# Kernel optimization log

Hardware: AMD Instinct MI355X
Metric: run time of the kernel (lower is better)

The kernel has to match this reference:

```python
import jax, jax.numpy as jnp
import numpy as np

BATCH = 1048576
IN_DIM = 64   # input_dim = A.shape[1]
OUT_DIM = 16  # output_dim = A.shape[0]


def setup_inputs() -> dict:
    key = jax.random.key(0)
    k1, k2, k3 = jax.random.split(key, 3)
    y = jax.random.normal(k1, (BATCH, IN_DIM), dtype=jnp.float32)
    A = jax.random.normal(k2, (OUT_DIM, IN_DIM), dtype=jnp.float32)
    b = jax.random.normal(k3, (BATCH, OUT_DIM), dtype=jnp.float32)
    return {"y": y, "A": A, "b": b}


def _block_matrix(A):
    # KKT block matrix [[2I, A^T], [A, 0]], shape (n+m, n+m); shared across batch.
    m, n = A.shape
    Id2 = 2.0 * jnp.eye(n, dtype=A.dtype)
    top = jnp.concatenate([Id2, A.T], axis=1)          # (n, n+m)
    bot = jnp.concatenate([A, jnp.zeros((m, m), A.dtype)], axis=1)  # (m, n+m)
    return jnp.concatenate([top, bot], axis=0)


def reference(y, A, b):
    # Solve block_matrix @ sol_i = [2*y_i; b_i] for all samples i in one batched solve
    # (original torch code loops torch.linalg.solve over the batch with the SAME matrix).
    n = A.shape[1]
    M = _block_matrix(A)                               # (n+m, n+m)
    rhs = jnp.concatenate([2.0 * y, b], axis=1)        # (batch, n+m)
    sol = jnp.linalg.solve(M, rhs.T).T                 # factorize once, all RHS at once
    y_star = sol[:, :n]
    return y_star
```

## Files before the change

kernel.cpp:

```cpp
#include <hip/hip_runtime.h>

#define BATCH   1048576
#define IN_DIM  64
#define OUT_DIM 16

__global__ __launch_bounds__(256) void precompute_kernel(
    const float* __restrict__ A, float* __restrict__ ws)
{
    __shared__ float sA[16][64];
    __shared__ float M[16][32];
    __shared__ float fac[16];
    __shared__ int piv;

    const int tid = threadIdx.x;

    for (int i = tid; i < 1024; i += 256) sA[i >> 6][i & 63] = A[i];
    __syncthreads();

    {
        const int i = tid >> 4, j = tid & 15;
        float s = 0.f;
        #pragma unroll
        for (int k = 0; k < 64; ++k) s = fmaf(sA[i][k], sA[j][k], s);
        M[i][j] = s;
        M[i][16 + j] = (i == j) ? 1.f : 0.f;
    }
    __syncthreads();

    for (int p = 0; p < 16; ++p) {
        if (tid == 0) {
            int best = p;
            float bv = fabsf(M[p][p]);
            for (int r = p + 1; r < 16; ++r) {
                float v = fabsf(M[r][p]);
                if (v > bv) { bv = v; best = r; }
            }
            piv = best;
        }
        __syncthreads();
        if (tid < 32) {
            const int pr = piv;
            if (pr != p) { float t = M[p][tid]; M[p][tid] = M[pr][tid]; M[pr][tid] = t; }
        }
        __syncthreads();
        const float pv = M[p][p];
        __syncthreads();
        if (tid < 32) M[p][tid] *= (1.0f / pv);
        __syncthreads();
        if (tid < 16) fac[tid] = M[tid][p];
        __syncthreads();
        for (int e = tid; e < 512; e += 256) {
            const int r = e >> 5, c = e & 31;
            if (r != p) M[r][c] = fmaf(-fac[r], M[p][c], M[r][c]);
        }
        __syncthreads();
    }

    for (int e = tid; e < 1024; e += 256) {
        const int k = e >> 4, j = e & 15;
        ws[e] = sA[j][k];
    }
    for (int e = tid; e < 1024; e += 256) {
        const int k = e >> 4, i = e & 15;
        float s = 0.f;
        #pragma unroll
        for (int j = 0; j < 16; ++j) s = fmaf(M[i][16 + j], sA[j][k], s);
        ws[1024 + e] = s;
    }
}

__global__ __launch_bounds__(256, 2) void apply_kernel(
    const float* __restrict__ y, const float* __restrict__ b,
    const float* __restrict__ ws, float* __restrict__ out)
{
    __shared__ float4 yT[4][64][16];

    const int tid = threadIdx.x;
    const int wv  = tid >> 6;
    const int l   = tid & 63;
    const size_t wbase = (size_t)blockIdx.x * 256 + (size_t)wv * 64;

    const float4* __restrict__ At4  = reinterpret_cast<const float4*>(ws);
    const float4* __restrict__ Ct4  = reinterpret_cast<const float4*>(ws + 1024);
    const float4* __restrict__ ysrc = reinterpret_cast<const float4*>(y) + wbase * 16;
    const float4* __restrict__ b4   = reinterpret_cast<const float4*>(b);
    float4* __restrict__ odst       = reinterpret_cast<float4*>(out) + wbase * 16;

    #pragma unroll
    for (int i = 0; i < 16; ++i) {
        const int f   = i * 64 + l;
        const int row = f >> 4, q = f & 15;
        yT[wv][row][q ^ (row & 15)] = ysrc[f];
    }

    float t[16];
    #pragma unroll
    for (int q = 0; q < 4; ++q) {
        const float4 bv = b4[(wbase + l) * 4 + q];
        t[4*q+0] = -bv.x; t[4*q+1] = -bv.y; t[4*q+2] = -bv.z; t[4*q+3] = -bv.w;
    }

    #pragma unroll
    for (int q = 0; q < 16; ++q) {
        const float4 yv = yT[wv][l][q ^ (l & 15)];
        #pragma unroll
        for (int dk = 0; dk < 4; ++dk) {
            const float yk = (dk == 0) ? yv.x : (dk == 1) ? yv.y :
                             (dk == 2) ? yv.z : yv.w;
            const int k = q * 4 + dk;
            #pragma unroll
            for (int jq = 0; jq < 4; ++jq) {
                const float4 a = At4[k * 4 + jq];
                t[4*jq+0] = fmaf(a.x, yk, t[4*jq+0]);
                t[4*jq+1] = fmaf(a.y, yk, t[4*jq+1]);
                t[4*jq+2] = fmaf(a.z, yk, t[4*jq+2]);
                t[4*jq+3] = fmaf(a.w, yk, t[4*jq+3]);
            }
        }
    }

    #pragma unroll
    for (int q = 0; q < 16; ++q) {
        float4 yv = yT[wv][l][q ^ (l & 15)];
        #pragma unroll
        for (int dk = 0; dk < 4; ++dk) {
            const int k = q * 4 + dk;
            float x = (dk == 0) ? yv.x : (dk == 1) ? yv.y :
                      (dk == 2) ? yv.z : yv.w;
            #pragma unroll
            for (int iq = 0; iq < 4; ++iq) {
                const float4 c = Ct4[k * 4 + iq];
                x = fmaf(-c.x, t[4*iq+0], x);
                x = fmaf(-c.y, t[4*iq+1], x);
                x = fmaf(-c.z, t[4*iq+2], x);
                x = fmaf(-c.w, t[4*iq+3], x);
            }
            if (dk == 0) yv.x = x; else if (dk == 1) yv.y = x;
            else if (dk == 2) yv.z = x; else yv.w = x;
        }
        yT[wv][l][q ^ (l & 15)] = yv;
    }

    #pragma unroll
    for (int i = 0; i < 16; ++i) {
        const int f   = i * 64 + l;
        const int row = f >> 4, q = f & 15;
        odst[f] = yT[wv][row][q ^ (row & 15)];
    }
}

extern "C" void kernel_launch(void* const* d_in, const int* in_sizes, int n_in,
                              void* d_out, int out_size, void* d_ws, size_t ws_size,
                              hipStream_t stream) {
    const float* y = (const float*)d_in[0];
    const float* A = (const float*)d_in[1];
    const float* b = (const float*)d_in[2];
    float* out = (float*)d_out;
    float* ws  = (float*)d_ws;

    precompute_kernel<<<1, 256, 0, stream>>>(A, ws);
    apply_kernel<<<BATCH / 256, 256, 0, stream>>>(y, b, ws, out);
}
```

Baseline: 163.7 us.

## Halve apply kernel LDS staging by processing y in two column halves

```diff
diff --git a/kernel.cpp b/kernel.cpp
--- a/kernel.cpp
+++ b/kernel.cpp
@@ -69,40 +69,50 @@
     }
 }
 
-__global__ __launch_bounds__(256, 2) void apply_kernel(
+__global__ __launch_bounds__(256, 5) void apply_kernel(
     const float* __restrict__ y, const float* __restrict__ b,
     const float* __restrict__ ws, float* __restrict__ out)
 {
-    __shared__ float4 yT[4][64][16];
+    __shared__ float4 buf[4][64][8];
 
     const int tid = threadIdx.x;
     const int wv  = tid >> 6;
     const int l   = tid & 63;
     const size_t wbase = (size_t)blockIdx.x * 256 + (size_t)wv * 64;
 
-    const float4* __restrict__ At4  = reinterpret_cast<const float4*>(ws);
-    const float4* __restrict__ Ct4  = reinterpret_cast<const float4*>(ws + 1024);
-    const float4* __restrict__ ysrc = reinterpret_cast<const float4*>(y) + wbase * 16;
-    const float4* __restrict__ b4   = reinterpret_cast<const float4*>(b);
-    float4* __restrict__ odst       = reinterpret_cast<float4*>(out) + wbase * 16;
-
-    #pragma unroll
-    for (int i = 0; i < 16; ++i) {
-        const int f   = i * 64 + l;
-        const int row = f >> 4, q = f & 15;
-        yT[wv][row][q ^ (row & 15)] = ysrc[f];
-    }
+    const float4* __restrict__ At4 = reinterpret_cast<const float4*>(ws);
+    const float4* __restrict__ Ct4 = reinterpret_cast<const float4*>(ws + 1024);
+    const float*  __restrict__ yb  = y   + wbase * 64;
+    float*        __restrict__ ob  = out + wbase * 64;
+    const float4* __restrict__ b4  = reinterpret_cast<const float4*>(b) + (wbase + l) * 4;
+
+    const int srow = l >> 3;
+    const int ssl  = l & 7;
 
     float t[16];
-    #pragma unroll
-    for (int q = 0; q < 4; ++q) {
-        const float4 bv = b4[(wbase + l) * 4 + q];
-        t[4*q+0] = -bv.x; t[4*q+1] = -bv.y; t[4*q+2] = -bv.z; t[4*q+3] = -bv.w;
-    }
-
-    #pragma unroll
-    for (int q = 0; q < 16; ++q) {
-        const float4 yv = yT[wv][l][q ^ (l & 15)];
+
+    {
+        float4 st[8];
+        #pragma unroll
+        for (int i = 0; i < 8; ++i) {
+            const int row = i * 8 + srow;
+            st[i] = *reinterpret_cast<const float4*>(yb + row * 64 + ssl * 4);
+        }
+        #pragma unroll
+        for (int q = 0; q < 4; ++q) {
+            const float4 bv = b4[q];
+            t[4*q+0] = -bv.x; t[4*q+1] = -bv.y; t[4*q+2] = -bv.z; t[4*q+3] = -bv.w;
+        }
+        #pragma unroll
+        for (int i = 0; i < 8; ++i) {
+            const int row = i * 8 + srow;
+            buf[wv][row][ssl ^ (row & 7)] = st[i];
+        }
+    }
+
+    #pragma unroll
+    for (int q = 0; q < 8; ++q) {
+        const float4 yv = buf[wv][l][q ^ (l & 7)];
         #pragma unroll
         for (int dk = 0; dk < 4; ++dk) {
             const float yk = (dk == 0) ? yv.x : (dk == 1) ? yv.y :
@@ -119,12 +129,46 @@
         }
     }
 
-    #pragma unroll
-    for (int q = 0; q < 16; ++q) {
-        float4 yv = yT[wv][l][q ^ (l & 15)];
-        #pragma unroll
-        for (int dk = 0; dk < 4; ++dk) {
-            const int k = q * 4 + dk;
+    {
+        float4 st[8];
+        #pragma unroll
+        for (int i = 0; i < 8; ++i) {
+            const int row = i * 8 + srow;
+            st[i] = *reinterpret_cast<const float4*>(yb + row * 64 + 32 + ssl * 4);
+        }
+        #pragma unroll
+        for (int i = 0; i < 8; ++i) {
+            const int row = i * 8 + srow;
+            buf[wv][row][ssl ^ (row & 7)] = st[i];
+        }
+    }
+
+    #pragma unroll
+    for (int q = 0; q < 8; ++q) {
+        const float4 yv = buf[wv][l][q ^ (l & 7)];
+        #pragma unroll
+        for (int dk = 0; dk < 4; ++dk) {
+            const float yk = (dk == 0) ? yv.x : (dk == 1) ? yv.y :
+                             (dk == 2) ? yv.z : yv.w;
+            const int k = 32 + q * 4 + dk;
+            #pragma unroll
+            for (int jq = 0; jq < 4; ++jq) {
+                const float4 a = At4[k * 4 + jq];
+                t[4*jq+0] = fmaf(a.x, yk, t[4*jq+0]);
+                t[4*jq+1] = fmaf(a.y, yk, t[4*jq+1]);
+                t[4*jq+2] = fmaf(a.z, yk, t[4*jq+2]);
+                t[4*jq+3] = fmaf(a.w, yk, t[4*jq+3]);
+            }
+        }
+    }
+
+    #pragma unroll
+    for (int q = 0; q < 8; ++q) {
+        const float4 yv = buf[wv][l][q ^ (l & 7)];
+        float xv[4];
+        #pragma unroll
+        for (int dk = 0; dk < 4; ++dk) {
+            const int k = 32 + q * 4 + dk;
             float x = (dk == 0) ? yv.x : (dk == 1) ? yv.y :
                       (dk == 2) ? yv.z : yv.w;
             #pragma unroll
@@ -135,17 +179,45 @@
                 x = fmaf(-c.z, t[4*iq+2], x);
                 x = fmaf(-c.w, t[4*iq+3], x);
             }
-            if (dk == 0) yv.x = x; else if (dk == 1) yv.y = x;
-            else if (dk == 2) yv.z = x; else yv.w = x;
-        }
-        yT[wv][l][q ^ (l & 15)] = yv;
-    }
-
-    #pragma unroll
-    for (int i = 0; i < 16; ++i) {
-        const int f   = i * 64 + l;
-        const int row = f >> 4, q = f & 15;
-        odst[f] = yT[wv][row][q ^ (row & 15)];
+            xv[dk] = x;
+        }
+        buf[wv][l][q ^ (l & 7)] = make_float4(xv[0], xv[1], xv[2], xv[3]);
+    }
+
+    #pragma unroll
+    for (int i = 0; i < 8; ++i) {
+        const int row = i * 8 + srow;
+        *reinterpret_cast<float4*>(ob + row * 64 + 32 + ssl * 4) =
+            buf[wv][row][ssl ^ (row & 7)];
+    }
+
+    #pragma unroll
+    for (int q = 0; q < 8; ++q) {
+        const float4 yv = *reinterpret_cast<const float4*>(yb + l * 64 + q * 4);
+        float xv[4];
+        #pragma unroll
+        for (int dk = 0; dk < 4; ++dk) {
+            const int k = q * 4 + dk;
+            float x = (dk == 0) ? yv.x : (dk == 1) ? yv.y :
+                      (dk == 2) ? yv.z : yv.w;
+            #pragma unroll
+            for (int iq = 0; iq < 4; ++iq) {
+                const float4 c = Ct4[k * 4 + iq];
+                x = fmaf(-c.x, t[4*iq+0], x);
+                x = fmaf(-c.y, t[4*iq+1], x);
+                x = fmaf(-c.z, t[4*iq+2], x);
+                x = fmaf(-c.w, t[4*iq+3], x);
+            }
+            xv[dk] = x;
+        }
+        buf[wv][l][q ^ (l & 7)] = make_float4(xv[0], xv[1], xv[2], xv[3]);
+    }
+
+    #pragma unroll
+    for (int i = 0; i < 8; ++i) {
+        const int row = i * 8 + srow;
+        *reinterpret_cast<float4*>(ob + row * 64 + ssl * 4) =
+            buf[wv][row][ssl ^ (row & 7)];
     }
 }
 
```

Measured after the change: 192.3 us. +17.5%, slower.

## Halve LDS staging buffer, keep y in registers, raise occupancy to 4 blocks

Applied to the files above, without the earlier changes.

```diff
diff --git a/kernel.cpp b/kernel.cpp
--- a/kernel.cpp
+++ b/kernel.cpp
@@ -69,44 +69,63 @@
     }
 }
 
-__global__ __launch_bounds__(256, 2) void apply_kernel(
+__global__ __launch_bounds__(256, 4) void apply_kernel(
     const float* __restrict__ y, const float* __restrict__ b,
     const float* __restrict__ ws, float* __restrict__ out)
 {
-    __shared__ float4 yT[4][64][16];
+    __shared__ float4 buf[4][64][8];
 
     const int tid = threadIdx.x;
     const int wv  = tid >> 6;
     const int l   = tid & 63;
     const size_t wbase = (size_t)blockIdx.x * 256 + (size_t)wv * 64;
 
-    const float4* __restrict__ At4  = reinterpret_cast<const float4*>(ws);
-    const float4* __restrict__ Ct4  = reinterpret_cast<const float4*>(ws + 1024);
-    const float4* __restrict__ ysrc = reinterpret_cast<const float4*>(y) + wbase * 16;
-    const float4* __restrict__ b4   = reinterpret_cast<const float4*>(b);
-    float4* __restrict__ odst       = reinterpret_cast<float4*>(out) + wbase * 16;
+    const float4* __restrict__ At4 = reinterpret_cast<const float4*>(ws);
+    const float4* __restrict__ Ct4 = reinterpret_cast<const float4*>(ws + 1024);
+    const float*  __restrict__ yb  = y   + wbase * 64;
+    float*        __restrict__ ob  = out + wbase * 64;
+    const float4* __restrict__ b4  = reinterpret_cast<const float4*>(b) + (wbase + l) * 4;
+
+    const int srow = l >> 3;
+    const int ssl  = l & 7;
+
+    float4 g0[8], g1[8];
+    #pragma unroll
+    for (int i = 0; i < 8; ++i)
+        g0[i] = *reinterpret_cast<const float4*>(yb + (i * 8 + srow) * 64 + ssl * 4);
+    #pragma unroll
+    for (int i = 0; i < 8; ++i)
+        g1[i] = *reinterpret_cast<const float4*>(yb + (i * 8 + srow) * 64 + 32 + ssl * 4);
+    const float4 bv0 = b4[0], bv1 = b4[1], bv2 = b4[2], bv3 = b4[3];
+
+    float t[16];
+    t[ 0] = -bv0.x; t[ 1] = -bv0.y; t[ 2] = -bv0.z; t[ 3] = -bv0.w;
+    t[ 4] = -bv1.x; t[ 5] = -bv1.y; t[ 6] = -bv1.z; t[ 7] = -bv1.w;
+    t[ 8] = -bv2.x; t[ 9] = -bv2.y; t[10] = -bv2.z; t[11] = -bv2.w;
+    t[12] = -bv3.x; t[13] = -bv3.y; t[14] = -bv3.z; t[15] = -bv3.w;
+
+    float4 yr[16];
 
     #pragma unroll
-    for (int i = 0; i < 16; ++i) {
-        const int f   = i * 64 + l;
-        const int row = f >> 4, q = f & 15;
-        yT[wv][row][q ^ (row & 15)] = ysrc[f];
-    }
+    for (int i = 0; i < 8; ++i)
+        buf[wv][i * 8 + srow][ssl ^ srow] = g0[i];
+    #pragma unroll
+    for (int s = 0; s < 8; ++s)
+        yr[s] = buf[wv][l][s ^ (l & 7)];
 
-    float t[16];
     #pragma unroll
-    for (int q = 0; q < 4; ++q) {
-        const float4 bv = b4[(wbase + l) * 4 + q];
-        t[4*q+0] = -bv.x; t[4*q+1] = -bv.y; t[4*q+2] = -bv.z; t[4*q+3] = -bv.w;
-    }
+    for (int i = 0; i < 8; ++i)
+        buf[wv][i * 8 + srow][ssl ^ srow] = g1[i];
+    #pragma unroll
+    for (int s = 0; s < 8; ++s)
+        yr[8 + s] = buf[wv][l][s ^ (l & 7)];
 
     #pragma unroll
     for (int q = 0; q < 16; ++q) {
-        const float4 yv = yT[wv][l][q ^ (l & 15)];
         #pragma unroll
         for (int dk = 0; dk < 4; ++dk) {
-            const float yk = (dk == 0) ? yv.x : (dk == 1) ? yv.y :
-                             (dk == 2) ? yv.z : yv.w;
+            const float yk = (dk == 0) ? yr[q].x : (dk == 1) ? yr[q].y :
+                             (dk == 2) ? yr[q].z : yr[q].w;
             const int k = q * 4 + dk;
             #pragma unroll
             for (int jq = 0; jq < 4; ++jq) {
@@ -121,12 +140,11 @@
 
     #pragma unroll
     for (int q = 0; q < 16; ++q) {
-        float4 yv = yT[wv][l][q ^ (l & 15)];
         #pragma unroll
         for (int dk = 0; dk < 4; ++dk) {
             const int k = q * 4 + dk;
-            float x = (dk == 0) ? yv.x : (dk == 1) ? yv.y :
-                      (dk == 2) ? yv.z : yv.w;
+            float x = (dk == 0) ? yr[q].x : (dk == 1) ? yr[q].y :
+                      (dk == 2) ? yr[q].z : yr[q].w;
             #pragma unroll
             for (int iq = 0; iq < 4; ++iq) {
                 const float4 c = Ct4[k * 4 + iq];
@@ -135,18 +153,28 @@
                 x = fmaf(-c.z, t[4*iq+2], x);
                 x = fmaf(-c.w, t[4*iq+3], x);
             }
-            if (dk == 0) yv.x = x; else if (dk == 1) yv.y = x;
-            else if (dk == 2) yv.z = x; else yv.w = x;
+            if      (dk == 0) yr[q].x = x;
+            else if (dk == 1) yr[q].y = x;
+            else if (dk == 2) yr[q].z = x;
+            else              yr[q].w = x;
         }
-        yT[wv][l][q ^ (l & 15)] = yv;
     }
 
     #pragma unroll
-    for (int i = 0; i < 16; ++i) {
-        const int f   = i * 64 + l;
-        const int row = f >> 4, q = f & 15;
-        odst[f] = yT[wv][row][q ^ (row & 15)];
-    }
+    for (int s = 0; s < 8; ++s)
+        buf[wv][l][s ^ (l & 7)] = yr[s];
+    #pragma unroll
+    for (int i = 0; i < 8; ++i)
+        *reinterpret_cast<float4*>(ob + (i * 8 + srow) * 64 + ssl * 4) =
+            buf[wv][i * 8 + srow][ssl ^ srow];
+
+    #pragma unroll
+    for (int s = 0; s < 8; ++s)
+        buf[wv][l][s ^ (l & 7)] = yr[8 + s];
+    #pragma unroll
+    for (int i = 0; i < 8; ++i)
+        *reinterpret_cast<float4*>(ob + (i * 8 + srow) * 64 + 32 + ssl * 4) =
+            buf[wv][i * 8 + srow][ssl ^ srow];
 }
 
 extern "C" void kernel_launch(void* const* d_in, const int* in_sizes, int n_in,
```

Result: slower. 246.3 us (+50.4%).
